# Kernel tuning notes

Hardware: AMD Instinct MI355X
Metric: run time of the kernel (lower is better)

## Reference

```python
import jax, jax.numpy as jnp
import numpy as np

N, CIN, COUT, K, H, W = 32, 64, 128, 4, 64, 64


def setup_inputs() -> dict:
    key = jax.random.key(0)
    k1, k2, k3, k4 = jax.random.split(key, 4)
    fan_in = CIN * K * K
    bound = 1.0 / np.sqrt(fan_in)
    x = jax.random.normal(k1, (N, CIN, H, W), dtype=jnp.float32)
    # kaiming_uniform-ish init scale for the conv-transpose weight (Cin, Cout, K, K)
    weight = jax.random.uniform(k2, (CIN, COUT, K, K), dtype=jnp.float32,
                                minval=-bound, maxval=bound)
    conv_bias = jax.random.uniform(k3, (COUT,), dtype=jnp.float32,
                                   minval=-bound, maxval=bound)
    extra_bias = jax.random.normal(k4, (COUT,), dtype=jnp.float32)
    return {"x": x, "weight": weight, "conv_bias": conv_bias, "extra_bias": extra_bias}


def reference(x, weight, conv_bias, extra_bias):
    # ConvTranspose2d(stride=1, pad=0) == conv with spatially flipped kernel and
    # full (K-1) padding. weight is torch IOHW (Cin,Cout,K,K) -> OIHW (Cout,Cin,K,K).
    k = weight.shape[2]
    w_oihw = jnp.flip(weight, (2, 3)).transpose(1, 0, 2, 3)
    y = jax.lax.conv_general_dilated(
        x, w_oihw,
        window_strides=(1, 1),
        padding=[(k - 1, k - 1), (k - 1, k - 1)],
        dimension_numbers=("NCHW", "OIHW", "NCHW"),
    )  # (N, Cout, H+K-1, W+K-1)
    pooled = y.mean(axis=(2, 3)) + conv_bias + extra_bias  # (N, Cout)
    out = 10.0 * jax.nn.logsumexp(pooled, axis=1, keepdims=True)  # (N, 1)
    return out
```

## Files before the change

### kernel.cpp

```cpp
#include <hip/hip_runtime.h>

#define Nn   32
#define CIN  64
#define COUT 128
#define HWVOL 4096
#define OHW_INV (1.0f/4489.0f)

__global__ __launch_bounds__(256) void sum_x_kernel(const float* __restrict__ x,
                                                    float* __restrict__ Sx) {
    const int g = blockIdx.x;
    const int t = threadIdx.x;
    const float4* xp = (const float4*)(x + (size_t)g * HWVOL);
    float acc = 0.0f;
#pragma unroll
    for (int j = 0; j < 4; ++j) {
        float4 v = xp[t + 256 * j];
        acc += (v.x + v.y) + (v.z + v.w);
    }
#pragma unroll
    for (int off = 32; off > 0; off >>= 1)
        acc += __shfl_down(acc, off, 64);
    __shared__ float part[4];
    if ((t & 63) == 0) part[t >> 6] = acc;
    __syncthreads();
    if (t == 0) Sx[g] = (part[0] + part[1]) + (part[2] + part[3]);
}

__global__ __launch_bounds__(256) void sum_w_kernel(const float* __restrict__ w,
                                                    float* __restrict__ Sw) {
    const int o = blockIdx.x * 256 + threadIdx.x;
    const float4* wp = (const float4*)(w + (size_t)o * 16);
    float4 a = wp[0], b = wp[1], c = wp[2], d = wp[3];
    Sw[o] = (((a.x + a.y) + (a.z + a.w)) + ((b.x + b.y) + (b.z + b.w))) +
            (((c.x + c.y) + (c.z + c.w)) + ((d.x + d.y) + (d.z + d.w)));
}

__global__ __launch_bounds__(128) void final_kernel(const float* __restrict__ Sx,
                                                    const float* __restrict__ Sw,
                                                    const float* __restrict__ conv_bias,
                                                    const float* __restrict__ extra_bias,
                                                    float* __restrict__ out) {
    const int n  = blockIdx.x;
    const int co = threadIdx.x;
    __shared__ float sxs[CIN];
    if (co < CIN) sxs[co] = Sx[n * CIN + co];
    __syncthreads();

    float acc = 0.0f;
#pragma unroll
    for (int ci = 0; ci < CIN; ++ci)
        acc = fmaf(sxs[ci], Sw[ci * COUT + co], acc);

    const float pooled = acc * OHW_INV + conv_bias[co] + extra_bias[co];

    __shared__ float red[COUT];
    red[co] = pooled;
    __syncthreads();
#pragma unroll
    for (int s = 64; s > 0; s >>= 1) {
        if (co < s) red[co] = fmaxf(red[co], red[co + s]);
        __syncthreads();
    }
    const float m = red[0];
    __syncthreads();
    red[co] = expf(pooled - m);
    __syncthreads();
#pragma unroll
    for (int s = 64; s > 0; s >>= 1) {
        if (co < s) red[co] += red[co + s];
        __syncthreads();
    }
    if (co == 0) out[n] = 10.0f * (m + logf(red[0]));
}

extern "C" void kernel_launch(void* const* d_in, const int* in_sizes, int n_in,
                              void* d_out, int out_size, void* d_ws, size_t ws_size,
                              hipStream_t stream) {
    const float* x          = (const float*)d_in[0];
    const float* weight     = (const float*)d_in[1];
    const float* conv_bias  = (const float*)d_in[2];
    const float* extra_bias = (const float*)d_in[3];
    float* out = (float*)d_out;

    float* Sx = (float*)d_ws;
    float* Sw = Sx + Nn * CIN;

    sum_x_kernel<<<Nn * CIN, 256, 0, stream>>>(x, Sx);
    sum_w_kernel<<<(CIN * COUT) / 256, 256, 0, stream>>>(weight, Sw);
    final_kernel<<<Nn, 128, 0, stream>>>(Sx, Sw, conv_bias, extra_bias, out);
}
```

Baseline: 81.24 us.

## Fuse three kernels into one with last-block-done finalization via atomic counter

Merges the x-plane sum, weight sum and final logsumexp kernels into one launch. Each block reduces its input plane, then bumps a global atomic counter, and the last block to finish does the weight reduction, the matvec and the logsumexp entirely in shared memory. A memset for the counter is added. This removes two kernel launches and their gaps, but the whole tail phase now runs serially on a single block, and the large shared-memory allocation may lower occupancy for the main reduction phase.

Result: slower. 148.2 us (+82.4%).

```diff
diff --git a/kernel.cpp b/kernel.cpp
--- a/kernel.cpp
+++ b/kernel.cpp
@@ -1,15 +1,24 @@
 #include <hip/hip_runtime.h>
 
-#define Nn   32
-#define CIN  64
-#define COUT 128
-#define HWVOL 4096
-#define OHW_INV (1.0f/4489.0f)
+#define Nn     32
+#define CIN    64
+#define COUT   128
+#define HWVOL  4096
+#define PLANES (Nn * CIN)
+#define OHW_INV (1.0f / 4489.0f)
 
-__global__ __launch_bounds__(256) void sum_x_kernel(const float* __restrict__ x,
-                                                    float* __restrict__ Sx) {
+__global__ __launch_bounds__(256) void fused_kernel(
+    const float* __restrict__ x,
+    const float* __restrict__ w,
+    const float* __restrict__ conv_bias,
+    const float* __restrict__ extra_bias,
+    float* __restrict__ Sx,
+    unsigned int* __restrict__ counter,
+    float* __restrict__ out)
+{
     const int g = blockIdx.x;
     const int t = threadIdx.x;
+
     const float4* xp = (const float4*)(x + (size_t)g * HWVOL);
     float acc = 0.0f;
 #pragma unroll
@@ -20,57 +29,74 @@
 #pragma unroll
     for (int off = 32; off > 0; off >>= 1)
         acc += __shfl_down(acc, off, 64);
+
     __shared__ float part[4];
+    __shared__ int   is_last;
     if ((t & 63) == 0) part[t >> 6] = acc;
     __syncthreads();
-    if (t == 0) Sx[g] = (part[0] + part[1]) + (part[2] + part[3]);
-}
+    if (t == 0) {
+        Sx[g] = (part[0] + part[1]) + (part[2] + part[3]);
+        __threadfence();
+        unsigned int old = atomicAdd(counter, 1u);
+        is_last = (old == PLANES - 1) ? 1 : 0;
+    }
+    __syncthreads();
+    if (!is_last) return;
+    __threadfence();
 
-__global__ __launch_bounds__(256) void sum_w_kernel(const float* __restrict__ w,
-                                                    float* __restrict__ Sw) {
-    const int o = blockIdx.x * 256 + threadIdx.x;
-    const float4* wp = (const float4*)(w + (size_t)o * 16);
-    float4 a = wp[0], b = wp[1], c = wp[2], d = wp[3];
-    Sw[o] = (((a.x + a.y) + (a.z + a.w)) + ((b.x + b.y) + (b.z + b.w))) +
-            (((c.x + c.y) + (c.z + c.w)) + ((d.x + d.y) + (d.z + d.w)));
-}
+    __shared__ float sw[CIN * COUT];
+    __shared__ float sxs[PLANES];
+    __shared__ float pooled[Nn * COUT];
+    __shared__ float bias[COUT];
 
-__global__ __launch_bounds__(128) void final_kernel(const float* __restrict__ Sx,
-                                                    const float* __restrict__ Sw,
-                                                    const float* __restrict__ conv_bias,
-                                                    const float* __restrict__ extra_bias,
-                                                    float* __restrict__ out) {
-    const int n  = blockIdx.x;
-    const int co = threadIdx.x;
-    __shared__ float sxs[CIN];
-    if (co < CIN) sxs[co] = Sx[n * CIN + co];
+#pragma unroll
+    for (int j = 0; j < PLANES / 256; ++j)
+        sxs[t + 256 * j] = Sx[t + 256 * j];
+    if (t < COUT) bias[t] = conv_bias[t] + extra_bias[t];
+#pragma unroll
+    for (int j = 0; j < (CIN * COUT) / 256; ++j) {
+        const int o = j * 256 + t;
+        const float4* wp = (const float4*)(w + (size_t)o * 16);
+        float4 a = wp[0], b = wp[1], c = wp[2], d = wp[3];
+        sw[o] = (((a.x + a.y) + (a.z + a.w)) + ((b.x + b.y) + (b.z + b.w))) +
+                (((c.x + c.y) + (c.z + c.w)) + ((d.x + d.y) + (d.z + d.w)));
+    }
     __syncthreads();
 
-    float acc = 0.0f;
 #pragma unroll
-    for (int ci = 0; ci < CIN; ++ci)
-        acc = fmaf(sxs[ci], Sw[ci * COUT + co], acc);
+    for (int j = 0; j < (Nn * COUT) / 256; ++j) {
+        const int idx = j * 256 + t;
+        const int n  = idx >> 7;
+        const int co = idx & (COUT - 1);
+        float a = 0.0f;
+#pragma unroll
+        for (int ci = 0; ci < CIN; ++ci)
+            a = fmaf(sxs[n * CIN + ci], sw[ci * COUT + co], a);
+        pooled[idx] = a * OHW_INV + bias[co];
+    }
+    __syncthreads();
 
-    const float pooled = acc * OHW_INV + conv_bias[co] + extra_bias[co];
-
-    __shared__ float red[COUT];
-    red[co] = pooled;
-    __syncthreads();
+    {
+        const int n = t >> 3;
+        const int r = t & 7;
+        float m = -3.4e38f, l = 0.0f;
 #pragma unroll
-    for (int s = 64; s > 0; s >>= 1) {
-        if (co < s) red[co] = fmaxf(red[co], red[co + s]);
-        __syncthreads();
+        for (int j = 0; j < 16; ++j) {
+            float v = pooled[n * COUT + r * 16 + j];
+            float mn = fmaxf(m, v);
+            l = l * __expf(m - mn) + __expf(v - mn);
+            m = mn;
+        }
+#pragma unroll
+        for (int off = 1; off < 8; off <<= 1) {
+            float m2 = __shfl_xor(m, off, 64);
+            float l2 = __shfl_xor(l, off, 64);
+            float mn = fmaxf(m, m2);
+            l = l * __expf(m - mn) + l2 * __expf(m2 - mn);
+            m = mn;
+        }
+        if (r == 0) out[n] = 10.0f * (m + logf(l));
     }
-    const float m = red[0];
-    __syncthreads();
-    red[co] = expf(pooled - m);
-    __syncthreads();
-#pragma unroll
-    for (int s = 64; s > 0; s >>= 1) {
-        if (co < s) red[co] += red[co + s];
-        __syncthreads();
-    }
-    if (co == 0) out[n] = 10.0f * (m + logf(red[0]));
 }
 
 extern "C" void kernel_launch(void* const* d_in, const int* in_sizes, int n_in,
@@ -83,9 +109,9 @@
     float* out = (float*)d_out;
 
     float* Sx = (float*)d_ws;
-    float* Sw = Sx + Nn * CIN;
+    unsigned int* counter = (unsigned int*)((char*)d_ws + PLANES * sizeof(float));
 
-    sum_x_kernel<<<Nn * CIN, 256, 0, stream>>>(x, Sx);
-    sum_w_kernel<<<(CIN * COUT) / 256, 256, 0, stream>>>(weight, Sw);
-    final_kernel<<<Nn, 128, 0, stream>>>(Sx, Sw, conv_bias, extra_bias, out);
+    hipMemsetAsync(counter, 0, sizeof(unsigned int), stream);
+    fused_kernel<<<PLANES, 256, 0, stream>>>(x, weight, conv_bias, extra_bias,
+                                             Sx, counter, out);
 }
```
